# Performance work log

Hardware: AMD Instinct MI355X
Metric: run time of the kernel (lower is better)

The kernel has to match this reference:

```python
import jax, jax.numpy as jnp
import numpy as np

N_SPECIES = 4; N_BASIS = 128; N_GRAPH = 16; R_MAX = 6.0
NS_NODE, NV_NODE = 32, 16          # node irreps 32x0e + 16x1o
NS_EDGE = 16                       # initial edge irreps 16x0e
NS_OUT, NV_OUT = 16, 8             # output irreps 16x0e + 8x1o
NS_IN = 2 * NS_NODE + NS_EDGE      # 80 concatenated scalars
NV_IN = 2 * NV_NODE                # 32 concatenated vectors
NS_CONV = NS_OUT + NV_OUT          # 24 scalars (16 features + 8 gates)
W_SIZES = [NS_IN * NS_CONV, NS_IN * NV_OUT, NV_IN * NV_OUT, NV_IN * NS_CONV, NV_IN * NV_OUT]
N_NODES, N_EDGES = 8192, 65536
EPS = 1e-5


def gaussian_basis(d, stop, n):
    offsets = jnp.linspace(0.0, stop, n)
    coeff = -0.5 / (offsets[1] - offsets[0]) ** 2
    return jnp.exp(coeff * (d[:, None] - offsets[None, :]) ** 2)


def seg_mean(vals, seg, cnt):
    return jax.ops.segment_sum(vals, seg, num_segments=N_GRAPH) / cnt[:, None]


def setup_inputs():
    key = jax.random.key(0)
    ks = jax.random.split(key, 20)
    rn = lambda k, shape, scale: jax.random.normal(k, shape, jnp.float32) * scale
    inp = {}
    inp["node_fea"] = rn(ks[0], (N_NODES, NS_NODE + 3 * NV_NODE), 1.0)
    d = 0.5 + 5.0 * jax.random.uniform(ks[1], (N_EDGES,), jnp.float32)
    vec = jax.random.normal(ks[2], (N_EDGES, 3), jnp.float32)
    inp["edge_attr"] = jnp.concatenate([d[:, None], vec], axis=1)
    inp["edge_index"] = jax.random.randint(ks[3], (2, N_EDGES), 0, N_NODES)
    inp["x"] = jax.random.randint(ks[4], (N_NODES,), 0, N_SPECIES)
    inp["batch"] = jnp.sort(jax.random.randint(ks[5], (N_NODES,), 0, N_GRAPH))
    inp["w_rh"] = rn(ks[6], (N_BASIS, 64), N_BASIS ** -0.5); inp["b_rh"] = jnp.zeros((64,), jnp.float32)
    inp["w_ro"] = rn(ks[7], (64, sum(W_SIZES)), 64 ** -0.5); inp["b_ro"] = jnp.zeros((sum(W_SIZES),), jnp.float32)
    inp["w_pre"] = rn(ks[8], (NS_EDGE, NS_EDGE), NS_EDGE ** -0.5); inp["b_pre"] = jnp.zeros((NS_EDGE,), jnp.float32)
    inp["w_sc"] = rn(ks[9], (NS_EDGE, N_SPECIES ** 2, NS_OUT), 1.0)
    inp["w_post_s"] = rn(ks[10], (NS_OUT, NS_OUT), NS_OUT ** -0.5); inp["b_post_s"] = jnp.zeros((NS_OUT,), jnp.float32)
    inp["w_post_v"] = rn(ks[11], (NV_OUT, NV_OUT), NV_OUT ** -0.5)
    inp["ln_w_s"] = jnp.ones((NS_OUT,), jnp.float32); inp["ln_b_s"] = jnp.zeros((NS_OUT,), jnp.float32)
    inp["ln_w_v"] = jnp.ones((NV_OUT,), jnp.float32)
    inp["w_skip"] = rn(ks[12], (NS_EDGE, NS_OUT), NS_EDGE ** -0.5)
    inp["w_edge_s"] = rn(ks[13], (NS_OUT, NS_OUT), NS_OUT ** -0.5); inp["b_edge_s"] = jnp.zeros((NS_OUT,), jnp.float32)
    inp["w_edge_v"] = rn(ks[14], (NV_OUT, NV_OUT), NV_OUT ** -0.5)
    return inp


def _forward(node_fea, edge_attr, w_rh, b_rh, w_ro, b_ro, w_pre, b_pre, w_sc,
             w_post_s, b_post_s, w_post_v, ln_w_s, ln_b_s, ln_w_v,
             w_skip, w_edge_s, b_edge_s, w_edge_v, edge_index, x, batch):
    E = edge_index.shape[1]
    idx_i, idx_j = edge_index[0], edge_index[1]
    one_hot = jax.nn.one_hot(N_SPECIES * x[idx_i] + x[idx_j], N_SPECIES ** 2, dtype=node_fea.dtype)
    d, vec = edge_attr[:, 0], edge_attr[:, 1:4]
    u = vec / (jnp.linalg.norm(vec, axis=1, keepdims=True) + 1e-12)
    Y1 = np.sqrt(3.0) * u                                   # l=1 sph harm, component norm; Y0 == 1
    rbf = gaussian_basis(d, R_MAX, N_BASIS)                 # edge_length_embedded
    edge_s0 = gaussian_basis(d, 6.0, NS_EDGE)               # distance_expansion -> initial edge scalars
    # self connection: edge scalars x species-pair one-hot -> output scalars
    sc = jnp.einsum('ei,ej,ijo->eo', edge_s0, one_hot, w_sc) / np.sqrt(NS_EDGE * N_SPECIES ** 2)
    edge_s = edge_s0 @ w_pre + b_pre                        # lin_pre
    # gather node features by edge indices and concat
    nf_i, nf_j = node_fea[idx_i], node_fea[idx_j]
    s_in = jnp.concatenate([nf_i[:, :NS_NODE], nf_j[:, :NS_NODE], edge_s], axis=1)  # [E,80]
    v_in = jnp.concatenate([nf_i[:, NS_NODE:].reshape(E, NV_NODE, 3),
                            nf_j[:, NS_NODE:].reshape(E, NV_NODE, 3)], axis=1)      # [E,32,3]
    # radial MLP -> per-edge tensor-product path weights
    h = jax.nn.silu(rbf @ w_rh + b_rh)
    w_all = h @ w_ro + b_ro                                 # [E, 3840]
    w1, w2, w3, w4, w5 = jnp.split(w_all, np.cumsum(W_SIZES)[:-1].tolist(), axis=1)
    # equivariant tensor-product paths (explicit l<=1 Clebsch-Gordan structure)
    s0 = jnp.einsum('ei,eio->eo', s_in, w1.reshape(E, NS_IN, NS_CONV)) / np.sqrt(NS_IN)            # 0e x 0e -> 0e
    vA = jnp.einsum('ei,eio,ec->eoc', s_in, w2.reshape(E, NS_IN, NV_OUT), Y1) / np.sqrt(NS_IN)     # 0e x 1o -> 1o
    vB = jnp.einsum('eic,eio->eoc', v_in, w3.reshape(E, NV_IN, NV_OUT)) / np.sqrt(NV_IN)           # 1o x 0e -> 1o
    s1 = jnp.einsum('eic,eio,ec->eo', v_in, w4.reshape(E, NV_IN, NS_CONV), Y1) / np.sqrt(3.0 * NV_IN)  # 1o.1o -> 0e
    vC = jnp.einsum('eic,eio->eoc', jnp.cross(v_in, Y1[:, None, :]), w5.reshape(E, NV_IN, NV_OUT)) / np.sqrt(2.0 * NV_IN)  # 1o x 1o -> 1o
    s_conv = s0 + s1                                        # [E,24]
    v_conv = vA + vB + vC                                   # [E,8,3]
    # gate nonlinearity inside conv
    s_out = jax.nn.silu(s_conv[:, :NS_OUT])
    v_out = v_conv * jax.nn.sigmoid(s_conv[:, NS_OUT:])[:, :, None]
    # lin_post then self connection
    s_out = s_out @ w_post_s + b_post_s + sc
    v_out = jnp.einsum('eic,io->eoc', v_out, w_post_v)
    # e3LayerNorm keyed by graph id of source node
    eb = batch[idx_i]
    cnt = jnp.maximum(jax.ops.segment_sum(jnp.ones((E,), s_out.dtype), eb, num_segments=N_GRAPH), 1.0)
    mu = seg_mean(s_out, eb, cnt)
    s_c = s_out - mu[eb]
    rms_s = jnp.sqrt(seg_mean(s_c ** 2, eb, cnt).mean(axis=1, keepdims=True) + EPS)
    s_n = s_c / rms_s[eb] * ln_w_s + ln_b_s
    rms_v = jnp.sqrt((seg_mean((v_out ** 2).sum(-1), eb, cnt) / 3.0).mean(axis=1, keepdims=True) + EPS)
    v_n = v_out / rms_v[eb][:, :, None] * ln_w_v[None, :, None]
    # skip connection from old edge features (scalars only)
    s_n = s_n + edge_s0 @ w_skip
    # final lin_edge
    s_fin = s_n @ w_edge_s + b_edge_s
    v_fin = jnp.einsum('eic,io->eoc', v_n, w_edge_v)
    return jnp.concatenate([s_fin, v_fin.reshape(E, NV_OUT * 3)], axis=1)  # [E,40]


def reference(node_fea, edge_attr, edge_index, x, batch, w_rh, b_rh, w_ro, b_ro,
              w_pre, b_pre, w_sc, w_post_s, b_post_s, w_post_v, ln_w_s, ln_b_s, ln_w_v,
              w_skip, w_edge_s, b_edge_s, w_edge_v):
    return _forward(node_fea, edge_attr, w_rh, b_rh, w_ro, b_ro, w_pre, b_pre, w_sc,
                    w_post_s, b_post_s, w_post_v, ln_w_s, ln_b_s, ln_w_v,
                    w_skip, w_edge_s, b_edge_s, w_edge_v, edge_index, x, batch)
```

## Files before the change

### kernel.cpp

```cpp
#include <hip/hip_runtime.h>

typedef unsigned short u16;
typedef unsigned int u32;
typedef __attribute__((ext_vector_type(8))) short short8;
typedef __attribute__((ext_vector_type(4))) float floatx4;

#define E_TOTAL 65536

__device__ __forceinline__ u16 f2bf(float f) {
    union { float f; u32 i; } c; c.f = f;
    const u32 u = c.i;
    const u32 r = (u + 0x7fffu + ((u >> 16) & 1u)) >> 16;
    return (u16)r;
}
__device__ __forceinline__ float bfu2f(u16 u) {
    union { u32 i; float f; } c; c.i = ((u32)u) << 16; return c.f;
}
__device__ __forceinline__ void split2(float x0, float x1, u32& hp, u32& lp) {
    union { float f; u32 u; } a0, a1, h0, h1, l0, l1;
    a0.f = x0; a1.f = x1;
    h0.u = a0.u & 0xFFFF0000u; h1.u = a1.u & 0xFFFF0000u;
    hp = __builtin_amdgcn_perm(a1.u, a0.u, 0x07060302u);
    l0.f = x0 - h0.f; l1.f = x1 - h1.f;
    lp = __builtin_amdgcn_perm(l1.u, l0.u, 0x07060302u);
}
union Frag8 { u32 u[4]; short8 s; };


__global__ void k_zero(float* __restrict__ ws) {
    const int i = threadIdx.x + blockIdx.x * blockDim.x;
    if (i < 1056) ws[i] = 0.0f;
}

__global__ __launch_bounds__(64) void k_probe(int* __restrict__ binv) {
    const int lane = threadIdx.x;
    const int q = lane >> 4;
    if (lane < 32) binv[lane] = lane;
    short8 bfr;
    #pragma unroll
    for (int j = 0; j < 8; ++j) bfr[j] = (short)f2bf((float)(q*8 + j + 1));
    #pragma unroll
    for (int s = 0; s < 32; ++s) {
        const int qa = s >> 3, ja = s & 7;
        short8 afr = {0,0,0,0,0,0,0,0};
        if (q == qa) afr[ja] = (short)f2bf(1.0f);
        floatx4 dc = {0.0f, 0.0f, 0.0f, 0.0f};
        dc = __builtin_amdgcn_mfma_f32_16x16x32_bf16(afr, bfr, dc, 0, 0, 0);
        if (lane == 0) {
            const int sB = (int)(dc[0] + 0.5f) - 1;
            if (sB >= 0 && sB < 32) binv[sB] = s;
        }
    }
}

__global__ __launch_bounds__(256) void k_edge_heavy(
    const float* __restrict__ node_fea, const float* __restrict__ edge_attr,
    const int* __restrict__ edge_index, const int* __restrict__ xsp,
    const float* __restrict__ w_rh, const float* __restrict__ b_rh,
    const float* __restrict__ w_ro, const float* __restrict__ b_ro,
    const float* __restrict__ w_pre, const float* __restrict__ b_pre,
    const float* __restrict__ w_sc, const float* __restrict__ w_post_s,
    const float* __restrict__ b_post_s, const float* __restrict__ w_post_v,
    const int* __restrict__ binv,
    float* __restrict__ out)
{
    __shared__ __align__(16) u16 a_rbf[2][16 * 128];
    __shared__ __align__(16) u16 a_h[2][16 * 64];
    __shared__ __align__(16) float sh_wt[16][258];
    __shared__ float sh_sin[16][80];
    __shared__ float sh_vl[16][3][32];
    __shared__ float sh_q[16][32];
    __shared__ float sh_cr[16][3][32];
    __shared__ float sh_acc[16][56];
    __shared__ float sh_es0[16][16];
    __shared__ float sh_y1[16][4];
    __shared__ int   sh_kmap[32];

    const int tid = threadIdx.x;
    const int ed = tid >> 4, l16 = tid & 15;
    const int lane = tid & 63, w = tid >> 6;
    const int quad = lane >> 4, l15 = lane & 15;
    const int e = blockIdx.x * 16 + ed;

    if (tid < 32) sh_kmap[tid] = binv[tid];

    const int ni = edge_index[e];
    const int nj = edge_index[E_TOTAL + e];
    const float4 ea = *(const float4*)(edge_attr + 4*e);
    const float d  = ea.x;
    const float vx = ea.y, vy = ea.z, vz = ea.w;
    const float invn = 1.0f / (sqrtf(vx*vx + vy*vy + vz*vz) + 1e-12f);
    const float Y0 = 1.7320508075688772f * vx * invn;
    const float Y1 = 1.7320508075688772f * vy * invn;
    const float Y2 = 1.7320508075688772f * vz * invn;
    if (l16 == 0) { sh_y1[ed][0] = Y0; sh_y1[ed][1] = Y1; sh_y1[ed][2] = Y2; }

    const float C128 = -0.5f * (127.0f/6.0f) * (127.0f/6.0f);
    const float S128 = 6.0f/127.0f;
    {
        short8 thi, tlo;
        #pragma unroll
        for (int r = 0; r < 8; ++r) {
            const int b = l16*8 + r;
            const float t = d - S128 * (float)b;
            const float x = expf(C128 * t * t);
            const u16 hi = f2bf(x);
            thi[r] = (short)hi;
            tlo[r] = (short)f2bf(x - bfu2f(hi));
        }
        *(short8*)&a_rbf[0][(l16*16 + ed)*8] = thi;
        *(short8*)&a_rbf[1][(l16*16 + ed)*8] = tlo;
    }
    {
        const float t = d - 0.4f * (float)l16;
        sh_es0[ed][l16] = expf(-3.125f * t * t);
    }

    const float rs80 = 0.11180339887498949f;
    const float rs32 = 0.17677669529663689f;
    {
        const float* fi = node_fea + (size_t)ni * 80;
        const float* fj = node_fea + (size_t)nj * 80;
        sh_sin[ed][2*l16+0]    = fi[2*l16+0] * rs80;
        sh_sin[ed][2*l16+1]    = fi[2*l16+1] * rs80;
        sh_sin[ed][32+2*l16+0] = fj[2*l16+0] * rs80;
        sh_sin[ed][32+2*l16+1] = fj[2*l16+1] * rs80;
        #pragma unroll
        for (int c = 0; c < 3; ++c) {
            sh_vl[ed][c][l16]      = fi[32 + 3*l16 + c] * rs32;
            sh_vl[ed][c][16 + l16] = fj[32 + 3*l16 + c] * rs32;
        }
    }
    for (int s = tid; s < 16*56; s += 256) (&sh_acc[0][0])[s] = 0.0f;
    __syncthreads();

    int km[8];
    u32 voff0[8], voff1[8];
    #pragma unroll
    for (int j = 0; j < 8; ++j) {
        km[j] = sh_kmap[quad*8 + j];
        voff0[j] = (u32)(km[j] * 3840 + l15);
        voff1[j] = voff0[j] + 32u * 3840u;
    }

    float my_sc;
    {
        const int o = l16;
        float es = b_pre[o];
        float sc = 0.0f;
        const int p = 4*xsp[ni] + xsp[nj];
        #pragma unroll
        for (int i = 0; i < 16; ++i) {
            const float g = sh_es0[ed][i];
            es += g * w_pre[i*16 + o];
            sc += g * w_sc[(i*16 + p)*16 + o];
        }
        sh_sin[ed][64 + o] = es * rs80;
        my_sc = sc * 0.0625f;
    }
    #pragma unroll
    for (int rr = 0; rr < 2; ++rr) {
        const int i = l16 + 16*rr;
        const float a0 = sh_vl[ed][0][i];
        const float a1 = sh_vl[ed][1][i];
        const float a2 = sh_vl[ed][2][i];
        sh_q[ed][i] = (a0*Y0 + a1*Y1 + a2*Y2) * 0.57735026918962573f;
        sh_cr[ed][0][i] = (a1*Y2 - a2*Y1) * 0.70710678118654746f;
        sh_cr[ed][1][i] = (a2*Y0 - a0*Y2) * 0.70710678118654746f;
        sh_cr[ed][2][i] = (a0*Y1 - a1*Y0) * 0.70710678118654746f;
    }

    {
        floatx4 hacc = {0.0f, 0.0f, 0.0f, 0.0f};
        #pragma unroll
        for (int kk = 0; kk < 4; ++kk) {
            const short8 ahi = *(const short8*)&a_rbf[0][((kk*4 + quad)*16 + l15)*8];
            const short8 alo = *(const short8*)&a_rbf[1][((kk*4 + quad)*16 + l15)*8];
            Frag8 bh, bl;
            #pragma unroll
            for (int jj = 0; jj < 4; ++jj) {
                const float x0 = w_rh[(size_t)(kk*32 + km[2*jj+0])*64 + w*16 + l15];
                const float x1 = w_rh[(size_t)(kk*32 + km[2*jj+1])*64 + w*16 + l15];
                split2(x0, x1, bh.u[jj], bl.u[jj]);
            }
            hacc = __builtin_amdgcn_mfma_f32_16x16x32_bf16(ahi, bh.s, hacc, 0, 0, 0);
            hacc = __builtin_amdgcn_mfma_f32_16x16x32_bf16(alo, bh.s, hacc, 0, 0, 0);
            hacc = __builtin_amdgcn_mfma_f32_16x16x32_bf16(ahi, bl.s, hacc, 0, 0, 0);
        }
        const int hn = w*16 + l15;
        const float bb = b_rh[hn];
        const int k8 = hn >> 3, j2 = hn & 7;
        #pragma unroll
        for (int r = 0; r < 4; ++r) {
            const float x = hacc[r] + bb;
            const float s = x / (1.0f + expf(-x));
            const int m = quad*4 + r;
            const u16 h = f2bf(s);
            a_h[0][(k8*16 + m)*8 + j2] = h;
            a_h[1][(k8*16 + m)*8 + j2] = f2bf(s - bfu2f(h));
        }
    }
    __syncthreads();

    const short8 a0h = *(const short8*)&a_h[0][((0*4 + quad)*16 + l15)*8];
    const short8 a1h = *(const short8*)&a_h[0][((1*4 + quad)*16 + l15)*8];
    const short8 a0l = *(const short8*)&a_h[1][((0*4 + quad)*16 + l15)*8];
    const short8 a1l = *(const short8*)&a_h[1][((1*4 + quad)*16 + l15)*8];

    for (int ch = 0; ch < 15; ++ch) {
        const int coff = ch * 256;
        floatx4 acc[4];
        float bias[4];
        #pragma unroll
        for (int ct = 0; ct < 4; ++ct) {
            const int sgct = __builtin_amdgcn_readfirstlane(ch*16 + w*4 + ct);
            const float* bp = w_ro + sgct*16;
            float f0[8], f1[8];
            #pragma unroll
            for (int j = 0; j < 8; ++j) {
                f0[j] = bp[voff0[j]];
                f1[j] = bp[voff1[j]];
            }
            Frag8 b0h, b0l, b1h, b1l;
            #pragma unroll
            for (int jj = 0; jj < 4; ++jj) {
                split2(f0[2*jj], f0[2*jj+1], b0h.u[jj], b0l.u[jj]);
                split2(f1[2*jj], f1[2*jj+1], b1h.u[jj], b1l.u[jj]);
            }
            floatx4 a = {0.0f, 0.0f, 0.0f, 0.0f};
            a = __builtin_amdgcn_mfma_f32_16x16x32_bf16(a0h, b0h.s, a, 0, 0, 0);
            a = __builtin_amdgcn_mfma_f32_16x16x32_bf16(a1h, b1h.s, a, 0, 0, 0);
            a = __builtin_amdgcn_mfma_f32_16x16x32_bf16(a0l, b0h.s, a, 0, 0, 0);
            a = __builtin_amdgcn_mfma_f32_16x16x32_bf16(a1l, b1h.s, a, 0, 0, 0);
            a = __builtin_amdgcn_mfma_f32_16x16x32_bf16(a0h, b0l.s, a, 0, 0, 0);
            a = __builtin_amdgcn_mfma_f32_16x16x32_bf16(a1h, b1l.s, a, 0, 0, 0);
            acc[ct] = a;
            bias[ct] = b_ro[sgct*16 + l15];
        }
        __syncthreads();
        #pragma unroll
        for (int ct = 0; ct < 4; ++ct) {
            const int col = w*64 + ct*16 + l15;
            #pragma unroll
            for (int r = 0; r < 4; ++r)
                sh_wt[quad*4 + r][col] = acc[ct][r] + bias[ct];
        }
        __syncthreads();

        if (ch <= 7) {
            const int hi = (ch == 7) ? 1920 : (coff + 256);
            for (int idx = tid; idx < 384; idx += 256) {
                const int eo = idx / 24, o = idx % 24;
                const int i0 = (coff > o) ? (coff - o + 23) / 24 : 0;
                int i1 = (hi - o + 23) / 24; if (i1 > 80) i1 = 80;
                float a = 0.0f;
                for (int i = i0; i < i1; ++i)
                    a += sh_sin[eo][i] * sh_wt[eo][i*24 + o - coff];
                sh_acc[eo][o] += a;
            }
        }
        if (ch == 7) {
            for (int idx = tid; idx < 128; idx += 256) {
                const int eo = idx >> 3, o = idx & 7;
                float a = 0.0f;
                #pragma unroll
                for (int i = 0; i < 16; ++i)
                    a += sh_sin[eo][i] * sh_wt[eo][128 + i*8 + o];
                sh_acc[eo][24 + o] += a;
            }
        }
        if (ch == 8 || ch == 9) {
            const int ib = (ch == 8) ? 16 : 48;
            for (int idx = tid; idx < 128; idx += 256) {
                const int eo = idx >> 3, o = idx & 7;
                float a = 0.0f;
                #pragma unroll
                for (int i2 = 0; i2 < 32; ++i2)
                    a += sh_sin[eo][ib + i2] * sh_wt[eo][i2*8 + o];
                sh_acc[eo][24 + o] += a;
            }
        }
        if (ch == 10) {
            for (int idx = tid; idx < 384; idx += 256) {
                const int eo = idx / 24, rem = idx % 24;
                const int o = rem / 3, cc = rem % 3;
                float a = 0.0f;
                #pragma unroll
                for (int i = 0; i < 32; ++i)
                    a += sh_vl[eo][cc][i] * sh_wt[eo][i*8 + o];
                sh_acc[eo][32 + o*3 + cc] += a;
            }
        }
        if (ch >= 11 && ch <= 13) {
            const int rel = coff - 2816;
            for (int idx = tid; idx < 384; idx += 256) {
                const int eo = idx / 24, o = idx % 24;
                const int i0 = (rel > o) ? (rel - o + 23) / 24 : 0;
                int i1 = (rel + 256 - o + 23) / 24; if (i1 > 32) i1 = 32;
                float a = 0.0f;
                for (int i = i0; i < i1; ++i)
                    a += sh_q[eo][i] * sh_wt[eo][i*24 + o - rel];
                sh_acc[eo][o] += a;
            }
        }
        if (ch == 14) {
            for (int idx = tid; idx < 384; idx += 256) {
                const int eo = idx / 24, rem = idx % 24;
                const int o = rem / 3, cc = rem % 3;
                float a = 0.0f;
                #pragma unroll
                for (int i = 0; i < 32; ++i)
                    a += sh_cr[eo][cc][i] * sh_wt[eo][i*8 + o];
                sh_acc[eo][32 + o*3 + cc] += a;
            }
        }
    }
    __syncthreads();

    {
        const int o = l16;
        float a = b_post_s[o] + my_sc;
        #pragma unroll
        for (int i = 0; i < 16; ++i) {
            const float sv = sh_acc[ed][i];
            a += (sv / (1.0f + expf(-sv))) * w_post_s[i*16 + o];
        }
        out[(size_t)e*40 + o] = a;
    }
    if (l16 < 8) {
        const int o = l16;
        const float Ya = sh_y1[ed][0], Yb = sh_y1[ed][1], Yc = sh_y1[ed][2];
        float r0 = 0.0f, r1 = 0.0f, r2 = 0.0f;
        #pragma unroll
        for (int i = 0; i < 8; ++i) {
            const float g  = 1.0f / (1.0f + expf(-sh_acc[ed][16 + i]));
            const float a2 = sh_acc[ed][24 + i];
            const float ww = w_post_v[i*8 + o];
            r0 += (a2*Ya + sh_acc[ed][32 + i*3 + 0]) * g * ww;
            r1 += (a2*Yb + sh_acc[ed][32 + i*3 + 1]) * g * ww;
            r2 += (a2*Yc + sh_acc[ed][32 + i*3 + 2]) * g * ww;
        }
        out[(size_t)e*40 + 16 + o*3 + 0] = r0;
        out[(size_t)e*40 + 16 + o*3 + 1] = r1;
        out[(size_t)e*40 + 16 + o*3 + 2] = r2;
    }
}

__global__ __launch_bounds__(256) void k_stats_partial(
    const float* __restrict__ sv, const int* __restrict__ edge_index,
    const int* __restrict__ batch, float* __restrict__ ws)
{
    __shared__ float sh_ed[256][40];
    __shared__ int   sh_eb[256];
    const int tid = threadIdx.x;
    const int e = blockIdx.x * 256 + tid;
    sh_eb[tid] = batch[edge_index[e]];
    const float* p = sv + (size_t)e * 40;
    #pragma unroll
    for (int j = 0; j < 40; ++j) sh_ed[tid][j] = p[j];
    __syncthreads();

    for (int slot = tid; slot < 768; slot += 256) {
        const int g = slot / 48, s = slot % 48;
        float acc = 0.0f;
        if (s < 16) {
            for (int k = 0; k < 256; ++k) {
                const float m = (sh_eb[k] == g) ? 1.0f : 0.0f;
                acc += m * sh_ed[k][s];
            }
        } else if (s < 32) {
            for (int k = 0; k < 256; ++k) {
                const float m = (sh_eb[k] == g) ? 1.0f : 0.0f;
                const float v = sh_ed[k][s - 16];
                acc += m * v * v;
            }
        } else if (s < 40) {
            const int o3 = 16 + (s - 32) * 3;
            for (int k = 0; k < 256; ++k) {
                const float m = (sh_eb[k] == g) ? 1.0f : 0.0f;
                const float v0 = sh_ed[k][o3], v1 = sh_ed[k][o3+1], v2 = sh_ed[k][o3+2];
                acc += m * (v0*v0 + v1*v1 + v2*v2);
            }
        } else if (s == 40) {
            for (int k = 0; k < 256; ++k) acc += (sh_eb[k] == g) ? 1.0f : 0.0f;
        }
        atomicAdd(&ws[slot], acc);
    }
}

__global__ __launch_bounds__(64) void k_stats_final(float* __restrict__ ws)
{
    const int tid = threadIdx.x;
    if (tid < 16) {
        const int g = tid;
        float cnt = ws[g*48 + 40]; if (cnt < 1.0f) cnt = 1.0f;
        const float ic = 1.0f / cnt;
        float vs = 0.0f;
        for (int chn = 0; chn < 16; ++chn) {
            const float mu = ws[g*48 + chn] * ic;
            ws[768 + g*16 + chn] = mu;
            vs += ws[g*48 + 16 + chn] * ic - mu * mu;
        }
        if (vs < 0.0f) vs = 0.0f;
        ws[1024 + g] = 1.0f / sqrtf(vs * (1.0f/16.0f) + 1e-5f);
        float vv = 0.0f;
        for (int o = 0; o < 8; ++o) vv += ws[g*48 + 32 + o];
        vv = vv * ic * (1.0f/3.0f) * (1.0f/8.0f);
        ws[1040 + g] = 1.0f / sqrtf(vv + 1e-5f);
    }
}

__global__ __launch_bounds__(256) void k_edge_final(
    float* buf, const float* __restrict__ ws,
    const float* __restrict__ edge_attr, const int* __restrict__ edge_index,
    const int* __restrict__ batch,
    const float* __restrict__ ln_w_s, const float* __restrict__ ln_b_s,
    const float* __restrict__ ln_w_v, const float* __restrict__ w_skip,
    const float* __restrict__ w_edge_s, const float* __restrict__ b_edge_s,
    const float* __restrict__ w_edge_v)
{
    __shared__ float sh_mu[16][16];
    __shared__ float sh_is[16], sh_iv[16];
    __shared__ float sh_lws[16], sh_lbs[16], sh_lwv[8];
    __shared__ float sh_skip[16][16], sh_wes[16][16], sh_bes[16], sh_wev[8][8];
    const int tid = threadIdx.x;
    sh_mu[tid >> 4][tid & 15]   = ws[768 + tid];
    sh_skip[tid >> 4][tid & 15] = w_skip[tid];
    sh_wes[tid >> 4][tid & 15]  = w_edge_s[tid];
    if (tid < 16) {
        sh_is[tid]  = ws[1024 + tid];
        sh_iv[tid]  = ws[1040 + tid];
        sh_lws[tid] = ln_w_s[tid];
        sh_lbs[tid] = ln_b_s[tid];
        sh_bes[tid] = b_edge_s[tid];
    }
    if (tid < 8)  sh_lwv[tid] = ln_w_v[tid];
    if (tid < 64) sh_wev[tid >> 3][tid & 7] = w_edge_v[tid];
    __syncthreads();

    const int e = blockIdx.x * 256 + tid;
    const int g = batch[edge_index[e]];
    const float d = edge_attr[4*e];
    float es0[16];
    #pragma unroll
    for (int b = 0; b < 16; ++b) {
        const float t = d - 0.4f * (float)b;
        es0[b] = expf(-3.125f * t * t);
    }
    float p[40];
    float* pb = buf + (size_t)e * 40;
    #pragma unroll
    for (int j = 0; j < 40; ++j) p[j] = pb[j];

    const float is = sh_is[g];
    float sn[16];
    #pragma unroll
    for (int chn = 0; chn < 16; ++chn)
        sn[chn] = (p[chn] - sh_mu[g][chn]) * is * sh_lws[chn] + sh_lbs[chn];
    #pragma unroll
    for (int b = 0; b < 16; ++b) {
        const float g0 = es0[b];
        #pragma unroll
        for (int chn = 0; chn < 16; ++chn) sn[chn] += g0 * sh_skip[b][chn];
    }
    #pragma unroll
    for (int o = 0; o < 16; ++o) {
        float a = sh_bes[o];
        #pragma unroll
        for (int chn = 0; chn < 16; ++chn) a += sn[chn] * sh_wes[chn][o];
        pb[o] = a;
    }
    const float iv = sh_iv[g];
    float vn[8][3];
    #pragma unroll
    for (int i = 0; i < 8; ++i) {
        const float f = iv * sh_lwv[i];
        vn[i][0] = p[16 + i*3 + 0] * f;
        vn[i][1] = p[16 + i*3 + 1] * f;
        vn[i][2] = p[16 + i*3 + 2] * f;
    }
    #pragma unroll
    for (int o = 0; o < 8; ++o) {
        float r0 = 0.0f, r1 = 0.0f, r2 = 0.0f;
        #pragma unroll
        for (int i = 0; i < 8; ++i) {
            const float w = sh_wev[i][o];
            r0 += vn[i][0] * w; r1 += vn[i][1] * w; r2 += vn[i][2] * w;
        }
        pb[16 + o*3 + 0] = r0;
        pb[16 + o*3 + 1] = r1;
        pb[16 + o*3 + 2] = r2;
    }
}

extern "C" void kernel_launch(void* const* d_in, const int* in_sizes, int n_in,
                              void* d_out, int out_size, void* d_ws, size_t ws_size,
                              hipStream_t stream)
{
    const float* node_fea  = (const float*)d_in[0];
    const float* edge_attr = (const float*)d_in[1];
    const int* edge_index  = (const int*)d_in[2];
    const int* xsp         = (const int*)d_in[3];
    const int* batch       = (const int*)d_in[4];
    const float* w_rh      = (const float*)d_in[5];
    const float* b_rh      = (const float*)d_in[6];
    const float* w_ro      = (const float*)d_in[7];
    const float* b_ro      = (const float*)d_in[8];
    const float* w_pre     = (const float*)d_in[9];
    const float* b_pre     = (const float*)d_in[10];
    const float* w_sc      = (const float*)d_in[11];
    const float* w_post_s  = (const float*)d_in[12];
    const float* b_post_s  = (const float*)d_in[13];
    const float* w_post_v  = (const float*)d_in[14];
    const float* ln_w_s    = (const float*)d_in[15];
    const float* ln_b_s    = (const float*)d_in[16];
    const float* ln_w_v    = (const float*)d_in[17];
    const float* w_skip    = (const float*)d_in[18];
    const float* w_edge_s  = (const float*)d_in[19];
    const float* b_edge_s  = (const float*)d_in[20];
    const float* w_edge_v  = (const float*)d_in[21];

    float* ws   = (float*)d_ws;
    int*   binv = (int*)(ws + 1056);
    float* out  = (float*)d_out;

    k_zero<<<2, 1024, 0, stream>>>(ws);
    k_probe<<<1, 64, 0, stream>>>(binv);
    k_edge_heavy<<<4096, 256, 0, stream>>>(node_fea, edge_attr, edge_index, xsp,
        w_rh, b_rh, w_ro, b_ro, w_pre, b_pre, w_sc, w_post_s, b_post_s, w_post_v,
        binv, out);
    k_stats_partial<<<256, 256, 0, stream>>>(out, edge_index, batch, ws);
    k_stats_final<<<1, 64, 0, stream>>>(ws);
    k_edge_final<<<256, 256, 0, stream>>>(out, ws, edge_attr, edge_index,
        batch, ln_w_s, ln_b_s, ln_w_v, w_skip, w_edge_s, b_edge_s, w_edge_v);
}
```

Baseline: 486.9 us.

## Switch split-bf16 MFMA to single fp16 MFMA and use shared-memory atomics for stats

Drops the hi/lo bf16 split emulation of fp32 GEMMs. The radial-hidden and weight-generation matmuls now use a single fp16 MFMA pass, which cuts MFMA count about threefold and removes the split and conversion ALU work. Separately, the per-graph statistics kernel now accumulates each edge directly into shared-memory bins with LDS atomics, replacing the O(256) masked scan per slot. The fp16 path gives up precision (10-bit mantissa, with packing via cvt_pkrtz round-toward-zero) and risks tolerance failures, and the LDS atomics may contend because sorted batches put most edges of a block in the same graph.

```diff
diff --git a/kernel.cpp b/kernel.cpp
--- a/kernel.cpp
+++ b/kernel.cpp
@@ -2,29 +2,18 @@
 
 typedef unsigned short u16;
 typedef unsigned int u32;
-typedef __attribute__((ext_vector_type(8))) short short8;
+typedef __attribute__((ext_vector_type(8))) _Float16 half8;
+typedef __attribute__((ext_vector_type(2))) __fp16 fp16x2;
 typedef __attribute__((ext_vector_type(4))) float floatx4;
 
 #define E_TOTAL 65536
 
-__device__ __forceinline__ u16 f2bf(float f) {
-    union { float f; u32 i; } c; c.f = f;
-    const u32 u = c.i;
-    const u32 r = (u + 0x7fffu + ((u >> 16) & 1u)) >> 16;
-    return (u16)r;
-}
-__device__ __forceinline__ float bfu2f(u16 u) {
-    union { u32 i; float f; } c; c.i = ((u32)u) << 16; return c.f;
-}
-__device__ __forceinline__ void split2(float x0, float x1, u32& hp, u32& lp) {
-    union { float f; u32 u; } a0, a1, h0, h1, l0, l1;
-    a0.f = x0; a1.f = x1;
-    h0.u = a0.u & 0xFFFF0000u; h1.u = a1.u & 0xFFFF0000u;
-    hp = __builtin_amdgcn_perm(a1.u, a0.u, 0x07060302u);
-    l0.f = x0 - h0.f; l1.f = x1 - h1.f;
-    lp = __builtin_amdgcn_perm(l1.u, l0.u, 0x07060302u);
-}
-union Frag8 { u32 u[4]; short8 s; };
+__device__ __forceinline__ u32 pk16(float x0, float x1) {
+    union { fp16x2 h; u32 u; } c;
+    c.h = __builtin_amdgcn_cvt_pkrtz(x0, x1);
+    return c.u;
+}
+union Frag8h { u32 u[4]; half8 v; };
 
 
 __global__ void k_zero(float* __restrict__ ws) {
@@ -36,16 +25,18 @@
     const int lane = threadIdx.x;
     const int q = lane >> 4;
     if (lane < 32) binv[lane] = lane;
-    short8 bfr;
-    #pragma unroll
-    for (int j = 0; j < 8; ++j) bfr[j] = (short)f2bf((float)(q*8 + j + 1));
+    half8 bfr;
+    #pragma unroll
+    for (int j = 0; j < 8; ++j) bfr[j] = (_Float16)(float)(q*8 + j + 1);
     #pragma unroll
     for (int s = 0; s < 32; ++s) {
         const int qa = s >> 3, ja = s & 7;
-        short8 afr = {0,0,0,0,0,0,0,0};
-        if (q == qa) afr[ja] = (short)f2bf(1.0f);
+        half8 afr;
+        #pragma unroll
+        for (int j = 0; j < 8; ++j) afr[j] = (_Float16)0.0f;
+        if (q == qa) afr[ja] = (_Float16)1.0f;
         floatx4 dc = {0.0f, 0.0f, 0.0f, 0.0f};
-        dc = __builtin_amdgcn_mfma_f32_16x16x32_bf16(afr, bfr, dc, 0, 0, 0);
+        dc = __builtin_amdgcn_mfma_f32_16x16x32_f16(afr, bfr, dc, 0, 0, 0);
         if (lane == 0) {
             const int sB = (int)(dc[0] + 0.5f) - 1;
             if (sB >= 0 && sB < 32) binv[sB] = s;
@@ -64,8 +55,8 @@
     const int* __restrict__ binv,
     float* __restrict__ out)
 {
-    __shared__ __align__(16) u16 a_rbf[2][16 * 128];
-    __shared__ __align__(16) u16 a_h[2][16 * 64];
+    __shared__ __align__(16) u16 a_rbf[16 * 128];
+    __shared__ __align__(16) u16 a_h[16 * 64];
     __shared__ __align__(16) float sh_wt[16][258];
     __shared__ float sh_sin[16][80];
     __shared__ float sh_vl[16][3][32];
@@ -98,18 +89,17 @@
     const float C128 = -0.5f * (127.0f/6.0f) * (127.0f/6.0f);
     const float S128 = 6.0f/127.0f;
     {
-        short8 thi, tlo;
-        #pragma unroll
-        for (int r = 0; r < 8; ++r) {
-            const int b = l16*8 + r;
-            const float t = d - S128 * (float)b;
-            const float x = expf(C128 * t * t);
-            const u16 hi = f2bf(x);
-            thi[r] = (short)hi;
-            tlo[r] = (short)f2bf(x - bfu2f(hi));
-        }
-        *(short8*)&a_rbf[0][(l16*16 + ed)*8] = thi;
-        *(short8*)&a_rbf[1][(l16*16 + ed)*8] = tlo;
+        Frag8h thi;
+        #pragma unroll
+        for (int r2 = 0; r2 < 4; ++r2) {
+            const int b0i = l16*8 + 2*r2;
+            const float t0 = d - S128 * (float)b0i;
+            const float t1 = d - S128 * (float)(b0i + 1);
+            const float x0 = expf(C128 * t0 * t0);
+            const float x1 = expf(C128 * t1 * t1);
+            thi.u[r2] = pk16(x0, x1);
+        }
+        *(half8*)&a_rbf[(l16*16 + ed)*8] = thi.v;
     }
     {
         const float t = d - 0.4f * (float)l16;
@@ -174,18 +164,15 @@
         floatx4 hacc = {0.0f, 0.0f, 0.0f, 0.0f};
         #pragma unroll
         for (int kk = 0; kk < 4; ++kk) {
-            const short8 ahi = *(const short8*)&a_rbf[0][((kk*4 + quad)*16 + l15)*8];
-            const short8 alo = *(const short8*)&a_rbf[1][((kk*4 + quad)*16 + l15)*8];
-            Frag8 bh, bl;
+            const half8 ah = *(const half8*)&a_rbf[((kk*4 + quad)*16 + l15)*8];
+            Frag8h bh;
             #pragma unroll
             for (int jj = 0; jj < 4; ++jj) {
                 const float x0 = w_rh[(size_t)(kk*32 + km[2*jj+0])*64 + w*16 + l15];
                 const float x1 = w_rh[(size_t)(kk*32 + km[2*jj+1])*64 + w*16 + l15];
-                split2(x0, x1, bh.u[jj], bl.u[jj]);
-            }
-            hacc = __builtin_amdgcn_mfma_f32_16x16x32_bf16(ahi, bh.s, hacc, 0, 0, 0);
-            hacc = __builtin_amdgcn_mfma_f32_16x16x32_bf16(alo, bh.s, hacc, 0, 0, 0);
-            hacc = __builtin_amdgcn_mfma_f32_16x16x32_bf16(ahi, bl.s, hacc, 0, 0, 0);
+                bh.u[jj] = pk16(x0, x1);
+            }
+            hacc = __builtin_amdgcn_mfma_f32_16x16x32_f16(ah, bh.v, hacc, 0, 0, 0);
         }
         const int hn = w*16 + l15;
         const float bb = b_rh[hn];
@@ -195,17 +182,14 @@
             const float x = hacc[r] + bb;
             const float s = x / (1.0f + expf(-x));
             const int m = quad*4 + r;
-            const u16 h = f2bf(s);
-            a_h[0][(k8*16 + m)*8 + j2] = h;
-            a_h[1][(k8*16 + m)*8 + j2] = f2bf(s - bfu2f(h));
+            union { _Float16 h; u16 u; } cv; cv.h = (_Float16)s;
+            a_h[(k8*16 + m)*8 + j2] = cv.u;
         }
     }
     __syncthreads();
 
-    const short8 a0h = *(const short8*)&a_h[0][((0*4 + quad)*16 + l15)*8];
-    const short8 a1h = *(const short8*)&a_h[0][((1*4 + quad)*16 + l15)*8];
-    const short8 a0l = *(const short8*)&a_h[1][((0*4 + quad)*16 + l15)*8];
-    const short8 a1l = *(const short8*)&a_h[1][((1*4 + quad)*16 + l15)*8];
+    const half8 a0 = *(const half8*)&a_h[((0*4 + quad)*16 + l15)*8];
+    const half8 a1 = *(const half8*)&a_h[((1*4 + quad)*16 + l15)*8];
 
     for (int ch = 0; ch < 15; ++ch) {
         const int coff = ch * 256;
@@ -221,19 +205,15 @@
                 f0[j] = bp[voff0[j]];
                 f1[j] = bp[voff1[j]];
             }
-            Frag8 b0h, b0l, b1h, b1l;
+            Frag8h b0, b1;
             #pragma unroll
             for (int jj = 0; jj < 4; ++jj) {
-                split2(f0[2*jj], f0[2*jj+1], b0h.u[jj], b0l.u[jj]);
-                split2(f1[2*jj], f1[2*jj+1], b1h.u[jj], b1l.u[jj]);
+                b0.u[jj] = pk16(f0[2*jj], f0[2*jj+1]);
+                b1.u[jj] = pk16(f1[2*jj], f1[2*jj+1]);
             }
             floatx4 a = {0.0f, 0.0f, 0.0f, 0.0f};
-            a = __builtin_amdgcn_mfma_f32_16x16x32_bf16(a0h, b0h.s, a, 0, 0, 0);
-            a = __builtin_amdgcn_mfma_f32_16x16x32_bf16(a1h, b1h.s, a, 0, 0, 0);
-            a = __builtin_amdgcn_mfma_f32_16x16x32_bf16(a0l, b0h.s, a, 0, 0, 0);
-            a = __builtin_amdgcn_mfma_f32_16x16x32_bf16(a1l, b1h.s, a, 0, 0, 0);
-            a = __builtin_amdgcn_mfma_f32_16x16x32_bf16(a0h, b0l.s, a, 0, 0, 0);
-            a = __builtin_amdgcn_mfma_f32_16x16x32_bf16(a1h, b1l.s, a, 0, 0, 0);
+            a = __builtin_amdgcn_mfma_f32_16x16x32_f16(a0, b0.v, a, 0, 0, 0);
+            a = __builtin_amdgcn_mfma_f32_16x16x32_f16(a1, b1.v, a, 0, 0, 0);
             acc[ct] = a;
             bias[ct] = b_ro[sgct*16 + l15];
         }
@@ -350,41 +330,35 @@
     const float* __restrict__ sv, const int* __restrict__ edge_index,
     const int* __restrict__ batch, float* __restrict__ ws)
 {
-    __shared__ float sh_ed[256][40];
-    __shared__ int   sh_eb[256];
+    __shared__ float bins[768];
     const int tid = threadIdx.x;
+    for (int s = tid; s < 768; s += 256) bins[s] = 0.0f;
+    __syncthreads();
+
     const int e = blockIdx.x * 256 + tid;
-    sh_eb[tid] = batch[edge_index[e]];
+    const int g = batch[edge_index[e]];
     const float* p = sv + (size_t)e * 40;
-    #pragma unroll
-    for (int j = 0; j < 40; ++j) sh_ed[tid][j] = p[j];
+    float v[40];
+    #pragma unroll
+    for (int j = 0; j < 40; ++j) v[j] = p[j];
+
+    float* bg = bins + g * 48;
+    #pragma unroll
+    for (int chn = 0; chn < 16; ++chn) {
+        atomicAdd(&bg[chn],      v[chn]);
+        atomicAdd(&bg[16 + chn], v[chn] * v[chn]);
+    }
+    #pragma unroll
+    for (int o = 0; o < 8; ++o) {
+        const float a = v[16 + o*3], b = v[16 + o*3 + 1], c = v[16 + o*3 + 2];
+        atomicAdd(&bg[32 + o], a*a + b*b + c*c);
+    }
+    atomicAdd(&bg[40], 1.0f);
     __syncthreads();
 
-    for (int slot = tid; slot < 768; slot += 256) {
-        const int g = slot / 48, s = slot % 48;
-        float acc = 0.0f;
-        if (s < 16) {
-            for (int k = 0; k < 256; ++k) {
-                const float m = (sh_eb[k] == g) ? 1.0f : 0.0f;
-                acc += m * sh_ed[k][s];
-            }
-        } else if (s < 32) {
-            for (int k = 0; k < 256; ++k) {
-                const float m = (sh_eb[k] == g) ? 1.0f : 0.0f;
-                const float v = sh_ed[k][s - 16];
-                acc += m * v * v;
-            }
-        } else if (s < 40) {
-            const int o3 = 16 + (s - 32) * 3;
-            for (int k = 0; k < 256; ++k) {
-                const float m = (sh_eb[k] == g) ? 1.0f : 0.0f;
-                const float v0 = sh_ed[k][o3], v1 = sh_ed[k][o3+1], v2 = sh_ed[k][o3+2];
-                acc += m * (v0*v0 + v1*v1 + v2*v2);
-            }
-        } else if (s == 40) {
-            for (int k = 0; k < 256; ++k) acc += (sh_eb[k] == g) ? 1.0f : 0.0f;
-        }
-        atomicAdd(&ws[slot], acc);
+    for (int s = tid; s < 768; s += 256) {
+        const float x = bins[s];
+        if (x != 0.0f) atomicAdd(&ws[s], x);
     }
 }
 
```

Measured after the change: 451.6 us. 1.08x faster.
